# Performance work log

Measured on AMD Instinct MI355X. Metric: run time of the kernel, lower is better.

The kernel has to match this reference:

```python
import jax, jax.numpy as jnp
import numpy as np

IN_DIM = 96
HIDDEN = 256
EPS = 1e-6
NEG = -1e10


def setup_inputs() -> dict:
    key = jax.random.key(0)
    ks = jax.random.split(key, 12)
    B, S = 8, 2048
    q = jax.random.normal(ks[0], (B, S, IN_DIM), dtype=jnp.float32)
    k = jax.random.normal(ks[1], (B, S, IN_DIM), dtype=jnp.float32)
    v = jax.random.normal(ks[2], (B, S, IN_DIM), dtype=jnp.float32)
    mask = jax.random.randint(ks[3], (B, S, S), 0, 2, dtype=jnp.int32)
    s = 1.0 / np.sqrt(IN_DIM)
    Wq = jax.random.normal(ks[4], (IN_DIM, HIDDEN), dtype=jnp.float32) * s
    bq = jax.random.normal(ks[5], (HIDDEN,), dtype=jnp.float32) * 0.01
    Wk = jax.random.normal(ks[6], (IN_DIM, HIDDEN), dtype=jnp.float32) * s
    bk = jax.random.normal(ks[7], (HIDDEN,), dtype=jnp.float32) * 0.01
    Wv = jax.random.normal(ks[8], (IN_DIM, HIDDEN), dtype=jnp.float32) * s
    bv = jax.random.normal(ks[9], (HIDDEN,), dtype=jnp.float32) * 0.01
    gamma = jnp.ones((HIDDEN,), dtype=jnp.float32)
    beta = jnp.zeros((HIDDEN,), dtype=jnp.float32)
    return {"query": q, "key": k, "value": v, "mask": mask,
            "Wq": Wq, "bq": bq, "Wk": Wk, "bk": bk, "Wv": Wv, "bv": bv,
            "gamma": gamma, "beta": beta}


def reference(query, key, value, mask, Wq, bq, Wk, bk, Wv, bv, gamma, beta):
    # Linear projections: [B,S,96] @ [96,H] -> [B,S,H]
    q = jnp.einsum('bsf,fh->bsh', query, Wq) + bq
    k = jnp.einsum('bsf,fh->bsh', key, Wk) + bk
    v = jnp.einsum('bsf,fh->bsh', value, Wv) + bv
    # Scaled dot-product scores: [B,S,S]
    score = jnp.einsum('bqh,bkh->bqk', q, k) / jnp.sqrt(jnp.float32(HIDDEN))
    score = jnp.where(mask == 0, jnp.float32(NEG), score)
    attn = jax.nn.softmax(score, axis=-1)
    out = jnp.einsum('bqk,bkh->bqh', attn, v)
    # LayerNorm over last dim, eps=1e-6
    mu = jnp.mean(out, axis=-1, keepdims=True)
    var = jnp.mean(jnp.square(out - mu), axis=-1, keepdims=True)
    normed = (out - mu) * jax.lax.rsqrt(var + EPS)
    return normed * gamma + beta
```

## Files before the change

kernel.cpp:

```cpp
#include <hip/hip_runtime.h>

#define B_   8
#define S_   2048
#define IN_  96
#define H_   256
#define NROW (B_ * S_)

typedef float    f32x4 __attribute__((ext_vector_type(4)));
typedef _Float16 f16x8 __attribute__((ext_vector_type(8)));
typedef int      i32x4 __attribute__((ext_vector_type(4)));

__device__ __forceinline__ unsigned short f2h(float x) {
    return __builtin_bit_cast(unsigned short, (_Float16)x);
}
__device__ __forceinline__ float h2f(unsigned short x) {
    return (float)__builtin_bit_cast(_Float16, x);
}
__device__ __forceinline__ void lds_barrier() {
    asm volatile("s_waitcnt lgkmcnt(0)\n\ts_barrier" ::: "memory");
}

__global__ __launch_bounds__(256) void wconv_kernel(
    const float* __restrict__ Wq, const float* __restrict__ Wk,
    const float* __restrict__ Wv, unsigned short* __restrict__ wt)
{
    const int p  = blockIdx.x >> 3;
    const int h0 = (blockIdx.x & 7) * 32;
    const float* W = (p == 0) ? Wq : (p == 1) ? Wk : Wv;
    unsigned short* dst = wt + (size_t)p * H_ * IN_ + (size_t)h0 * IN_;

    __shared__ unsigned short lds[32][100];
    const int t = threadIdx.x;
    #pragma unroll
    for (int i = 0; i < 12; ++i) {
        int idx = i * 256 + t;
        int f = idx >> 5;
        int hl = idx & 31;
        lds[hl][f] = f2h(W[f * H_ + h0 + hl]);
    }
    __syncthreads();
    #pragma unroll
    for (int j = 0; j < 6; ++j) {
        int e = (j * 256 + t) * 2;
        int hl = e / IN_, f = e % IN_;
        unsigned int pk = (unsigned int)lds[hl][f] |
                          ((unsigned int)lds[hl][f + 1] << 16);
        ((unsigned int*)dst)[j * 256 + t] = pk;
    }
}

__global__ __launch_bounds__(256) void maskpack_kernel(
    const int* __restrict__ mask, unsigned* __restrict__ pm32)
{
    __shared__ unsigned char nib[4][8][64];
    const int wave = threadIdx.x >> 6;
    const int lane = threadIdx.x & 63;
    const int wid  = blockIdx.x * 4 + wave;
    const int r0   = wid * 2;

    const int* m0 = mask + (size_t)r0 * S_ + lane * 4;
    const int* m1 = m0 + S_;
    i32x4 a[8], b[8];
    #pragma unroll
    for (int j = 0; j < 8; ++j)
        a[j] = __builtin_nontemporal_load((const i32x4*)(m0 + j * 256));
    #pragma unroll
    for (int j = 0; j < 8; ++j)
        b[j] = __builtin_nontemporal_load((const i32x4*)(m1 + j * 256));

    #pragma unroll
    for (int j = 0; j < 8; ++j) {
        unsigned n0 = (a[j][0] != 0 ? 1u : 0u) | (a[j][1] != 0 ? 2u : 0u)
                    | (a[j][2] != 0 ? 4u : 0u) | (a[j][3] != 0 ? 8u : 0u);
        unsigned n1 = (b[j][0] != 0 ? 1u : 0u) | (b[j][1] != 0 ? 2u : 0u)
                    | (b[j][2] != 0 ? 4u : 0u) | (b[j][3] != 0 ? 8u : 0u);
        nib[wave][j][lane] = (unsigned char)(n0 | (n1 << 4));
    }
    asm volatile("s_waitcnt lgkmcnt(0)" ::: "memory");

    unsigned long long v = *(const unsigned long long*)
        &nib[wave][lane >> 3][(lane & 7) * 8];
    unsigned long long x0 = v & 0x0F0F0F0F0F0F0F0FULL;
    unsigned long long x1 = (v >> 4) & 0x0F0F0F0F0F0F0F0FULL;
    x0 = (x0 | (x0 >> 4))  & 0x00FF00FF00FF00FFULL;
    x1 = (x1 | (x1 >> 4))  & 0x00FF00FF00FF00FFULL;
    x0 = (x0 | (x0 >> 8))  & 0x0000FFFF0000FFFFULL;
    x1 = (x1 | (x1 >> 8))  & 0x0000FFFF0000FFFFULL;
    x0 = (x0 | (x0 >> 16)) & 0xFFFFFFFFULL;
    x1 = (x1 | (x1 >> 16)) & 0xFFFFFFFFULL;

    pm32[(size_t)r0 * 64 + lane]       = (unsigned)x0;
    pm32[(size_t)(r0 + 1) * 64 + lane] = (unsigned)x1;
}

__global__ __launch_bounds__(256) void proj_kernel3(
    const float* __restrict__ query, const float* __restrict__ key,
    const float* __restrict__ value, const unsigned short* __restrict__ wt,
    const float* __restrict__ bq, const float* __restrict__ bk,
    const float* __restrict__ bv,
    unsigned short* __restrict__ pq, unsigned short* __restrict__ pk,
    unsigned short* __restrict__ pv)
{
    __shared__ unsigned short Xs[3][16][104];

    const int t    = threadIdx.x;
    const int lane = t & 63;
    const int wave = t >> 6;
    const int col  = lane & 15;
    const int quad = lane >> 4;
    const int bi   = blockIdx.x;
    const int s0   = bi * 16;
    const int b    = s0 >> 11;
    const int sl   = s0 & (S_ - 1);

    const float* srcs[3] = { query + (size_t)s0 * IN_,
                             key   + (size_t)s0 * IN_,
                             value + (size_t)s0 * IN_ };
    #pragma unroll
    for (int p = 0; p < 3; ++p) {
        #pragma unroll
        for (int i = 0; i < 2; ++i) {
            int idx = i * 256 + t;
            if (idx < 384) {
                f32x4 x = *(const f32x4*)(srcs[p] + idx * 4);
                int r = idx / 24;
                int f = (idx - r * 24) * 4;
                unsigned long long pkk =
                    (unsigned long long)f2h(x[0])
                  | ((unsigned long long)f2h(x[1]) << 16)
                  | ((unsigned long long)f2h(x[2]) << 32)
                  | ((unsigned long long)f2h(x[3]) << 48);
                *(unsigned long long*)&Xs[p][r][f] = pkk;
            }
        }
    }
    __syncthreads();

    const int hc = wave;
    #pragma unroll
    for (int p = 0; p < 3; ++p) {
        const unsigned short* wbase = wt + (size_t)p * H_ * IN_;
        f16x8 wfr[4][3];
        #pragma unroll
        for (int ht = 0; ht < 4; ++ht)
            #pragma unroll
            for (int kc = 0; kc < 3; ++kc)
                wfr[ht][kc] = *(const f16x8*)(wbase
                    + (size_t)(hc * 64 + ht * 16 + col) * IN_ + kc * 32 + quad * 8);
        f16x8 xfr[3];
        #pragma unroll
        for (int kc = 0; kc < 3; ++kc)
            xfr[kc] = *(const f16x8*)&Xs[p][col][kc * 32 + quad * 8];

        f32x4 acc[4];
        #pragma unroll
        for (int ht = 0; ht < 4; ++ht) acc[ht] = (f32x4)(0.0f);
        #pragma unroll
        for (int kc = 0; kc < 3; ++kc)
            #pragma unroll
            for (int ht = 0; ht < 4; ++ht)
                acc[ht] = (p < 2)
                    ? __builtin_amdgcn_mfma_f32_16x16x32_f16(xfr[kc], wfr[ht][kc], acc[ht], 0, 0, 0)
                    : __builtin_amdgcn_mfma_f32_16x16x32_f16(wfr[ht][kc], xfr[kc], acc[ht], 0, 0, 0);

        if (p < 2) {
            unsigned short* dst  = (p == 0) ? pq : pk;
            const float*    bias = (p == 0) ? bq : bk;
            #pragma unroll
            for (int ht = 0; ht < 4; ++ht) {
                float bh = bias[hc * 64 + ht * 16 + col];
                const int s    = hc * 2 + (ht >> 1);
                const int lq   = ((ht & 1) * 2 + (col >> 3)) * 16;
                const int j    = col & 7;
                #pragma unroll
                for (int r = 0; r < 4; ++r)
                    dst[(size_t)(((bi * 8 + s) * 64 + lq + quad * 4 + r)) * 8 + j]
                        = f2h(acc[ht][r] + bh);
            }
        } else {
            const int kl  = (sl & 63) + col;
            const int c   = sl >> 6;
            const int s2  = kl >> 5;
            const int qv  = (kl >> 3) & 3;
            const int jj  = col & 7;
            #pragma unroll
            for (int ht = 0; ht < 4; ++ht) {
                f32x4 b4 = *(const f32x4*)(bv + hc * 64 + ht * 16 + quad * 4);
                #pragma unroll
                for (int r = 0; r < 4; ++r)
                    pv[(size_t)(((b * 32 + c) * 32 + hc * 8 + ht * 2 + s2) * 64
                                + qv * 16 + quad * 4 + r) * 8 + jj]
                        = f2h(acc[ht][r] + b4[r]);
            }
        }
    }
}

__global__ __launch_bounds__(256, 3) void attn_kernel(
    const unsigned short* __restrict__ pq, const unsigned short* __restrict__ pk,
    const unsigned short* __restrict__ pv, const unsigned long long* __restrict__ pm,
    unsigned short* __restrict__ Opart, float* __restrict__ lpart)
{
    __shared__ __align__(16) unsigned short Qs[8192];
    __shared__ unsigned short P[2][32][68];
    __shared__ float lsum[4][32];

    const int tid  = threadIdx.x;
    const int wave = tid >> 6;
    const int lane = tid & 63;
    const int col  = lane & 15;
    const int quad = lane >> 4;

    const int b     = blockIdx.x & 7;
    const int strip = (blockIdx.x >> 3) & 63;
    const int kh    = blockIdx.x >> 9;
    const int q0    = strip << 5;

    {
        const unsigned short* qsrc = pq + (size_t)(b * 128 + strip * 2) * 4096;
        #pragma unroll
        for (int ph = 0; ph < 4; ++ph) {
            int i = ph * 2048 + tid * 8;
            *(f16x8*)&Qs[i] = *(const f16x8*)(qsrc + i);
        }
    }

    f32x4 O[2][4];
    #pragma unroll
    for (int st = 0; st < 2; ++st)
        #pragma unroll
        for (int ht = 0; ht < 4; ++ht) O[st][ht] = (f32x4)(0.0f);
    float l0 = 0.0f, l1 = 0.0f;

    const unsigned short* pkb = pk + (size_t)(b * 128) * 4096 + lane * 8;
    const unsigned short* pvb = pv + (size_t)(b * 32) * 32 * 512
                                   + (size_t)wave * 8 * 512 + lane * 8;

    const unsigned* pm32 = (const unsigned*)pm;
    const int sh = (wave & 1) * 16 + quad * 4;
    const unsigned* mp0 = pm32 + (size_t)(b * S_ + q0 + col) * 64
                        + kh * 16 + (wave >> 1);
    const unsigned* mp1 = mp0 + 16 * 64;

    f16x8 kf[8];
    #pragma unroll
    for (int s = 0; s < 8; ++s)
        kf[s] = *(const f16x8*)(pkb + (size_t)(kh * 32 + wave) * 4096 + s * 512);

    unsigned mw0 = mp0[0];
    unsigned mw1 = mp1[0];

    __syncthreads();

    #pragma unroll 2
    for (int c = 0; c < 8; ++c) {
        const int pb = c & 1;
        const int cn = (c < 7) ? c + 1 : c;
        const int gc = kh * 8 + c;

        const unsigned short* vb = pvb + (size_t)gc * 32 * 512;
        f16x8 vf[4][2];
        #pragma unroll
        for (int ht = 0; ht < 4; ++ht)
            #pragma unroll
            for (int s2 = 0; s2 < 2; ++s2)
                vf[ht][s2] = *(const f16x8*)(vb + (size_t)(ht * 2 + s2) * 512);

        unsigned mn0 = mp0[cn * 2];
        unsigned mn1 = mp1[cn * 2];

        f32x4 St0 = (f32x4)(0.0f), St1 = (f32x4)(0.0f);
        __builtin_amdgcn_s_setprio(1);
        #pragma unroll
        for (int s = 0; s < 8; ++s) {
            f16x8 q0f = *(const f16x8*)&Qs[s * 512 + lane * 8];
            f16x8 q1f = *(const f16x8*)&Qs[4096 + s * 512 + lane * 8];
            St0 = __builtin_amdgcn_mfma_f32_16x16x32_f16(kf[s], q0f, St0, 0, 0, 0);
            St1 = __builtin_amdgcn_mfma_f32_16x16x32_f16(kf[s], q1f, St1, 0, 0, 0);
        }
        __builtin_amdgcn_s_setprio(0);

        {
            const unsigned short* kb = pkb + (size_t)(kh * 32 + cn * 4 + wave) * 4096;
            #pragma unroll
            for (int s = 0; s < 8; ++s)
                kf[s] = *(const f16x8*)(kb + s * 512);
        }

        {
            unsigned bits = mw0 >> sh;
            unsigned long long pk64 = 0;
            #pragma unroll
            for (int r = 0; r < 4; ++r) {
                float e = exp2f(fmaf(St0[r], 0.0901679843f, -8.65617025f));
                float p = ((bits >> r) & 1u) ? e : 0.0f;
                _Float16 ph = (_Float16)p;
                l0 += (float)ph;
                pk64 |= (unsigned long long)__builtin_bit_cast(unsigned short, ph)
                        << (16 * r);
            }
            *(unsigned long long*)&P[pb][col][wave * 16 + quad * 4] = pk64;
        }
        {
            unsigned bits = mw1 >> sh;
            unsigned long long pk64 = 0;
            #pragma unroll
            for (int r = 0; r < 4; ++r) {
                float e = exp2f(fmaf(St1[r], 0.0901679843f, -8.65617025f));
                float p = ((bits >> r) & 1u) ? e : 0.0f;
                _Float16 ph = (_Float16)p;
                l1 += (float)ph;
                pk64 |= (unsigned long long)__builtin_bit_cast(unsigned short, ph)
                        << (16 * r);
            }
            *(unsigned long long*)&P[pb][16 + col][wave * 16 + quad * 4] = pk64;
        }
        mw0 = mn0; mw1 = mn1;

        lds_barrier();

        __builtin_amdgcn_s_setprio(1);
        #pragma unroll
        for (int st = 0; st < 2; ++st) {
            #pragma unroll
            for (int s2 = 0; s2 < 2; ++s2) {
                union { unsigned long long u[2]; f16x8 v; } pu;
                const unsigned short* pr = &P[pb][st * 16 + col][s2 * 32 + quad * 8];
                pu.u[0] = *(const unsigned long long*)pr;
                pu.u[1] = *(const unsigned long long*)(pr + 4);
                f16x8 pf = pu.v;
                #pragma unroll
                for (int ht = 0; ht < 4; ++ht)
                    O[st][ht] = __builtin_amdgcn_mfma_f32_16x16x32_f16(pf, vf[ht][s2], O[st][ht], 0, 0, 0);
            }
        }
        __builtin_amdgcn_s_setprio(0);
    }

    l0 += __shfl_xor(l0, 16); l0 += __shfl_xor(l0, 32);
    l1 += __shfl_xor(l1, 16); l1 += __shfl_xor(l1, 32);
    if (lane < 16) { lsum[wave][lane] = l0; lsum[wave][16 + lane] = l1; }
    __syncthreads();

    if (wave == 0 && lane < 16) {
        #pragma unroll
        for (int st = 0; st < 2; ++st) {
            float lt = lsum[0][st * 16 + lane] + lsum[1][st * 16 + lane]
                     + lsum[2][st * 16 + lane] + lsum[3][st * 16 + lane];
            lpart[(size_t)kh * NROW + b * S_ + q0 + st * 16 + lane] = lt;
        }
    }

    unsigned short* OT = Qs;
    #pragma unroll
    for (int st = 0; st < 2; ++st)
        #pragma unroll
        for (int ht = 0; ht < 4; ++ht)
            #pragma unroll
            for (int r = 0; r < 4; ++r)
                OT[(st * 16 + quad * 4 + r) * 256 + wave * 64 + ht * 16 + col]
                    = f2h(O[st][ht][r]);
    __syncthreads();

    unsigned short* ob = Opart + (size_t)kh * NROW * H_
                       + (size_t)(b * S_ + q0) * H_;
    const int rrow = tid >> 3;
    const int hof  = (tid & 7) * 32;
    #pragma unroll
    for (int j = 0; j < 4; ++j)
        *(f16x8*)(ob + (size_t)rrow * H_ + hof + j * 8)
            = *(const f16x8*)(OT + rrow * 256 + hof + j * 8);
}

__global__ __launch_bounds__(256) void merge_ln_kernel(
    const unsigned short* __restrict__ Opart, const float* __restrict__ lpart,
    const float* __restrict__ gamma, const float* __restrict__ beta,
    float* __restrict__ out)
{
    const int row  = blockIdx.x * 4 + (threadIdx.x >> 6);
    const int lane = threadIdx.x & 63;

    float linv = 1.0f / (lpart[row] + lpart[NROW + row]
                       + lpart[2 * NROW + row] + lpart[3 * NROW + row]);

    const unsigned short* o0 = Opart + (size_t)row * H_ + lane * 4;
    unsigned long long a0 = *(const unsigned long long*)o0;
    unsigned long long a1 = *(const unsigned long long*)(o0 + (size_t)NROW * H_);
    unsigned long long a2 = *(const unsigned long long*)(o0 + (size_t)2 * NROW * H_);
    unsigned long long a3 = *(const unsigned long long*)(o0 + (size_t)3 * NROW * H_);

    float vals[4];
    float sum = 0.0f;
    #pragma unroll
    for (int j = 0; j < 4; ++j) {
        vals[j] = (h2f((unsigned short)(a0 >> (16 * j)))
                 + h2f((unsigned short)(a1 >> (16 * j)))
                 + h2f((unsigned short)(a2 >> (16 * j)))
                 + h2f((unsigned short)(a3 >> (16 * j)))) * linv;
        sum += vals[j];
    }
    sum += __shfl_xor(sum, 1);  sum += __shfl_xor(sum, 2);
    sum += __shfl_xor(sum, 4);  sum += __shfl_xor(sum, 8);
    sum += __shfl_xor(sum, 16); sum += __shfl_xor(sum, 32);
    float mu = sum * (1.0f / H_);

    float sq = 0.0f;
    #pragma unroll
    for (int j = 0; j < 4; ++j) {
        float d = vals[j] - mu;
        sq += d * d;
    }
    sq += __shfl_xor(sq, 1);  sq += __shfl_xor(sq, 2);
    sq += __shfl_xor(sq, 4);  sq += __shfl_xor(sq, 8);
    sq += __shfl_xor(sq, 16); sq += __shfl_xor(sq, 32);
    float rstd = rsqrtf(sq * (1.0f / H_) + 1e-6f);

    f32x4 g  = *(const f32x4*)(gamma + lane * 4);
    f32x4 be = *(const f32x4*)(beta  + lane * 4);
    f32x4 o;
    #pragma unroll
    for (int j = 0; j < 4; ++j)
        o[j] = (vals[j] - mu) * rstd * g[j] + be[j];
    *(f32x4*)(out + (size_t)row * H_ + lane * 4) = o;
}

extern "C" void kernel_launch(void* const* d_in, const int* in_sizes, int n_in,
                              void* d_out, int out_size, void* d_ws, size_t ws_size,
                              hipStream_t stream)
{
    const float* query = (const float*)d_in[0];
    const float* key   = (const float*)d_in[1];
    const float* value = (const float*)d_in[2];
    const int*   mask  = (const int*)d_in[3];
    const float* Wq = (const float*)d_in[4];
    const float* bq = (const float*)d_in[5];
    const float* Wk = (const float*)d_in[6];
    const float* bk = (const float*)d_in[7];
    const float* Wv = (const float*)d_in[8];
    const float* bv = (const float*)d_in[9];
    const float* gamma = (const float*)d_in[10];
    const float* beta  = (const float*)d_in[11];
    float* out = (float*)d_out;

    const size_t NQK = (size_t)B_ * S_ * H_;
    unsigned short* pq = (unsigned short*)d_ws;
    unsigned short* pk = pq + NQK;
    unsigned short* pv = pk + NQK;
    unsigned short* wt = pv + NQK;
    unsigned short* Op = wt + (size_t)3 * H_ * IN_;
    float*          lp = (float*)(Op + (size_t)4 * NROW * H_);
    unsigned long long* pm = (unsigned long long*)(lp + 4 * NROW);

    wconv_kernel<<<24, 256, 0, stream>>>(Wq, Wk, Wv, wt);
    maskpack_kernel<<<2048, 256, 0, stream>>>(mask, (unsigned*)pm);
    proj_kernel3<<<B_ * S_ / 16, 256, 0, stream>>>(query, key, value, wt,
                                                   bq, bk, bv, pq, pk, pv);
    attn_kernel<<<B_ * S_ / 32 * 4, 256, 0, stream>>>(pq, pk, pv, pm, Op, lp);
    merge_ln_kernel<<<NROW / 4, 256, 0, stream>>>(Op, lp, gamma, beta, out);
}
```

Before: 316.7 us.

## Software-pipeline QK scores one chunk ahead of PV in attention loop

Restructures the attention chunk loop so the QK^T scores and exp for chunk i+1 are computed before the PV MFMAs for chunk i, using the double-buffered P tile. A prologue handles the first chunk and an epilogue handles the last PV. This lets the exp/VALU work and the PV matrix work of adjacent chunks overlap across the single barrier per iteration. K prefetch now runs two chunks ahead. The output copy loop is also remapped so consecutive threads write contiguous row segments, giving more coalesced stores. The costs are extra code size and register pressure, plus a different barrier placement that must stay correct.

```diff
diff --git a/kernel.cpp b/kernel.cpp
--- a/kernel.cpp
+++ b/kernel.cpp
@@ -247,28 +247,12 @@
     for (int s = 0; s < 8; ++s)
         kf[s] = *(const f16x8*)(pkb + (size_t)(kh * 32 + wave) * 4096 + s * 512);
 
-    unsigned mw0 = mp0[0];
-    unsigned mw1 = mp1[0];
-
-    __syncthreads();
-
-    #pragma unroll 2
-    for (int c = 0; c < 8; ++c) {
-        const int pb = c & 1;
-        const int cn = (c < 7) ? c + 1 : c;
-        const int gc = kh * 8 + c;
-
-        const unsigned short* vb = pvb + (size_t)gc * 32 * 512;
-        f16x8 vf[4][2];
-        #pragma unroll
-        for (int ht = 0; ht < 4; ++ht)
-            #pragma unroll
-            for (int s2 = 0; s2 < 2; ++s2)
-                vf[ht][s2] = *(const f16x8*)(vb + (size_t)(ht * 2 + s2) * 512);
-
-        unsigned mn0 = mp0[cn * 2];
-        unsigned mn1 = mp1[cn * 2];
-
+    unsigned mc0 = mp0[0];
+    unsigned mc1 = mp1[0];
+
+    lds_barrier();
+
+    {
         f32x4 St0 = (f32x4)(0.0f), St1 = (f32x4)(0.0f);
         __builtin_amdgcn_s_setprio(1);
         #pragma unroll
@@ -281,14 +265,16 @@
         __builtin_amdgcn_s_setprio(0);
 
         {
-            const unsigned short* kb = pkb + (size_t)(kh * 32 + cn * 4 + wave) * 4096;
+            const unsigned short* kb = pkb + (size_t)(kh * 32 + 4 + wave) * 4096;
             #pragma unroll
             for (int s = 0; s < 8; ++s)
                 kf[s] = *(const f16x8*)(kb + s * 512);
         }
+        unsigned mn0 = mp0[2];
+        unsigned mn1 = mp1[2];
 
         {
-            unsigned bits = mw0 >> sh;
+            unsigned bits = mc0 >> sh;
             unsigned long long pk64 = 0;
             #pragma unroll
             for (int r = 0; r < 4; ++r) {
@@ -299,10 +285,10 @@
                 pk64 |= (unsigned long long)__builtin_bit_cast(unsigned short, ph)
                         << (16 * r);
             }
-            *(unsigned long long*)&P[pb][col][wave * 16 + quad * 4] = pk64;
+            *(unsigned long long*)&P[0][col][wave * 16 + quad * 4] = pk64;
         }
         {
-            unsigned bits = mw1 >> sh;
+            unsigned bits = mc1 >> sh;
             unsigned long long pk64 = 0;
             #pragma unroll
             for (int r = 0; r < 4; ++r) {
@@ -313,11 +299,76 @@
                 pk64 |= (unsigned long long)__builtin_bit_cast(unsigned short, ph)
                         << (16 * r);
             }
-            *(unsigned long long*)&P[pb][16 + col][wave * 16 + quad * 4] = pk64;
-        }
-        mw0 = mn0; mw1 = mn1;
+            *(unsigned long long*)&P[0][16 + col][wave * 16 + quad * 4] = pk64;
+        }
+        mc0 = mn0; mc1 = mn1;
 
         lds_barrier();
+    }
+
+    #pragma unroll 2
+    for (int i = 0; i < 7; ++i) {
+        const int pb  = i & 1;
+        const int cn2 = (i < 5) ? i + 2 : 7;
+        const int gc  = kh * 8 + i;
+
+        const unsigned short* vb = pvb + (size_t)gc * 32 * 512;
+        f16x8 vf[4][2];
+        #pragma unroll
+        for (int ht = 0; ht < 4; ++ht)
+            #pragma unroll
+            for (int s2 = 0; s2 < 2; ++s2)
+                vf[ht][s2] = *(const f16x8*)(vb + (size_t)(ht * 2 + s2) * 512);
+
+        f32x4 St0 = (f32x4)(0.0f), St1 = (f32x4)(0.0f);
+        __builtin_amdgcn_s_setprio(1);
+        #pragma unroll
+        for (int s = 0; s < 8; ++s) {
+            f16x8 q0f = *(const f16x8*)&Qs[s * 512 + lane * 8];
+            f16x8 q1f = *(const f16x8*)&Qs[4096 + s * 512 + lane * 8];
+            St0 = __builtin_amdgcn_mfma_f32_16x16x32_f16(kf[s], q0f, St0, 0, 0, 0);
+            St1 = __builtin_amdgcn_mfma_f32_16x16x32_f16(kf[s], q1f, St1, 0, 0, 0);
+        }
+        __builtin_amdgcn_s_setprio(0);
+
+        {
+            const unsigned short* kb = pkb + (size_t)(kh * 32 + cn2 * 4 + wave) * 4096;
+            #pragma unroll
+            for (int s = 0; s < 8; ++s)
+                kf[s] = *(const f16x8*)(kb + s * 512);
+        }
+        unsigned mn0 = mp0[cn2 * 2];
+        unsigned mn1 = mp1[cn2 * 2];
+
+        {
+            unsigned bits = mc0 >> sh;
+            unsigned long long pk64 = 0;
+            #pragma unroll
+            for (int r = 0; r < 4; ++r) {
+                float e = exp2f(fmaf(St0[r], 0.0901679843f, -8.65617025f));
+                float p = ((bits >> r) & 1u) ? e : 0.0f;
+                _Float16 ph = (_Float16)p;
+                l0 += (float)ph;
+                pk64 |= (unsigned long long)__builtin_bit_cast(unsigned short, ph)
+                        << (16 * r);
+            }
+            *(unsigned long long*)&P[pb ^ 1][col][wave * 16 + quad * 4] = pk64;
+        }
+        {
+            unsigned bits = mc1 >> sh;
+            unsigned long long pk64 = 0;
+            #pragma unroll
+            for (int r = 0; r < 4; ++r) {
+                float e = exp2f(fmaf(St1[r], 0.0901679843f, -8.65617025f));
+                float p = ((bits >> r) & 1u) ? e : 0.0f;
+                _Float16 ph = (_Float16)p;
+                l1 += (float)ph;
+                pk64 |= (unsigned long long)__builtin_bit_cast(unsigned short, ph)
+                        << (16 * r);
+            }
+            *(unsigned long long*)&P[pb ^ 1][16 + col][wave * 16 + quad * 4] = pk64;
+        }
+        mc0 = mn0; mc1 = mn1;
 
         __builtin_amdgcn_s_setprio(1);
         #pragma unroll
@@ -335,6 +386,34 @@
             }
         }
         __builtin_amdgcn_s_setprio(0);
+
+        lds_barrier();
+    }
+
+    {
+        const unsigned short* vb = pvb + (size_t)(kh * 8 + 7) * 32 * 512;
+        f16x8 vf[4][2];
+        #pragma unroll
+        for (int ht = 0; ht < 4; ++ht)
+            #pragma unroll
+            for (int s2 = 0; s2 < 2; ++s2)
+                vf[ht][s2] = *(const f16x8*)(vb + (size_t)(ht * 2 + s2) * 512);
+        __builtin_amdgcn_s_setprio(1);
+        #pragma unroll
+        for (int st = 0; st < 2; ++st) {
+            #pragma unroll
+            for (int s2 = 0; s2 < 2; ++s2) {
+                union { unsigned long long u[2]; f16x8 v; } pu;
+                const unsigned short* pr = &P[1][st * 16 + col][s2 * 32 + quad * 8];
+                pu.u[0] = *(const unsigned long long*)pr;
+                pu.u[1] = *(const unsigned long long*)(pr + 4);
+                f16x8 pf = pu.v;
+                #pragma unroll
+                for (int ht = 0; ht < 4; ++ht)
+                    O[st][ht] = __builtin_amdgcn_mfma_f32_16x16x32_f16(pf, vf[ht][s2], O[st][ht], 0, 0, 0);
+            }
+        }
+        __builtin_amdgcn_s_setprio(0);
     }
 
     l0 += __shfl_xor(l0, 16); l0 += __shfl_xor(l0, 32);
@@ -364,12 +443,14 @@
 
     unsigned short* ob = Opart + (size_t)kh * NROW * H_
                        + (size_t)(b * S_ + q0) * H_;
-    const int rrow = tid >> 3;
-    const int hof  = (tid & 7) * 32;
-    #pragma unroll
-    for (int j = 0; j < 4; ++j)
-        *(f16x8*)(ob + (size_t)rrow * H_ + hof + j * 8)
-            = *(const f16x8*)(OT + rrow * 256 + hof + j * 8);
+    const int r8 = tid >> 5;
+    const int c8 = (tid & 31) * 8;
+    #pragma unroll
+    for (int j = 0; j < 4; ++j) {
+        const int row = j * 8 + r8;
+        *(f16x8*)(ob + (size_t)row * H_ + c8)
+            = *(const f16x8*)(OT + row * 256 + c8);
+    }
 }
 
 __global__ __launch_bounds__(256) void merge_ln_kernel(
```

Result: faster. 307.0 us (-3.1%).
